# Kernel tuning notes

Hardware: AMD Instinct MI355X
Metric: run time of the kernel (lower is better)

The kernel has to match this reference:

```python
import jax, jax.numpy as jnp
import numpy as np

SEQ = 512      # sentence length n
WD, TD = 100, 28
IN = WD + TD   # 128, lstm input size == hidden size
H = IN         # 128
D = 2 * H      # 256, biLSTM output per token
MLP_IN = 2 * D # 512
HID = MLP_IN   # 512, MLP hidden (hidden_size=mlpInputSize)
V, T = 50000, 50


def setup_inputs() -> dict:
    key = jax.random.key(0)
    keys = iter(jax.random.split(key, 64))
    def nrm(shape, s=0.1):
        return jax.random.normal(next(keys), shape, jnp.float32) * s
    inp = {}
    inp["word_ids"] = jax.random.randint(next(keys), (SEQ,), 0, V)
    inp["tag_ids"] = jax.random.randint(next(keys), (SEQ,), 0, T)
    inp["word_emb_table"] = nrm((V, WD))
    inp["tag_emb_table"] = nrm((T, TD))
    # initHiddenCellState: randn, layout [layer*2+dir, hidden] (batch=1 squeezed)
    inp["h0"] = nrm((4, H), 1.0)
    inp["c0"] = nrm((4, H), 1.0)
    # 2-layer biLSTM params; layer0 input IN, layer1 input 2*H
    for l, insz in ((0, IN), (1, 2 * H)):
        for d in ("f", "b"):
            inp[f"Wih_l{l}{d}"] = nrm((4 * H, insz))
            inp[f"Whh_l{l}{d}"] = nrm((4 * H, H))
            inp[f"bih_l{l}{d}"] = nrm((4 * H,))
            inp[f"bhh_l{l}{d}"] = nrm((4 * H,))
    # MLP: Linear(MLP_IN, HID) -> tanh -> Linear(HID, 1)
    inp["W1"] = nrm((HID, MLP_IN))
    inp["b1"] = nrm((HID,))
    inp["W2"] = nrm((1, HID))
    inp["b2"] = nrm((1,))
    return inp


def _run_dir(x, Wih, Whh, bih, bhh, h0, c0, rev):
    # x: [S, in]; returns hidden states [S, H]
    xs = x[::-1] if rev else x
    pre = xs @ Wih.T + bih + bhh  # precompute input contribution [S, 4H]
    def step(carry, p):
        h, c = carry
        g = p + h @ Whh.T
        i, f, gg, o = jnp.split(g, 4)
        i, f, o = jax.nn.sigmoid(i), jax.nn.sigmoid(f), jax.nn.sigmoid(o)
        c = f * c + i * jnp.tanh(gg)
        h = o * jnp.tanh(c)
        return (h, c), h
    _, hs = jax.lax.scan(step, (h0, c0), pre)
    return hs[::-1] if rev else hs


def reference(word_ids, tag_ids, word_emb_table, tag_emb_table, h0, c0,
              Wih_l0f, Whh_l0f, bih_l0f, bhh_l0f,
              Wih_l0b, Whh_l0b, bih_l0b, bhh_l0b,
              Wih_l1f, Whh_l1f, bih_l1f, bhh_l1f,
              Wih_l1b, Whh_l1b, bih_l1b, bhh_l1b,
              W1, b1, W2, b2):
    # embed + concat: [S, IN]
    x = jnp.concatenate([word_emb_table[word_ids], tag_emb_table[tag_ids]], axis=1)
    layers = [((Wih_l0f, Whh_l0f, bih_l0f, bhh_l0f), (Wih_l0b, Whh_l0b, bih_l0b, bhh_l0b)),
              ((Wih_l1f, Whh_l1f, bih_l1f, bhh_l1f), (Wih_l1b, Whh_l1b, bih_l1b, bhh_l1b))]
    h = x
    for l, (pf, pb) in enumerate(layers):
        hf = _run_dir(h, *pf, h0[2 * l], c0[2 * l], False)
        hb = _run_dir(h, *pb, h0[2 * l + 1], c0[2 * l + 1], True)
        h = jnp.concatenate([hf, hb], axis=1)  # [S, 2H]
    # batched pairwise MLP: score(i,j) = W2 @ tanh(W1 @ [h_i; h_j] + b1) + b2
    W1a, W1b = W1[:, :D], W1[:, D:]
    A = h @ W1a.T  # [S, HID]
    B = h @ W1b.T  # [S, HID]
    hmid = jnp.tanh(A[:, None, :] + B[None, :, :] + b1)  # [S, S, HID]
    scores = jnp.einsum('nmh,h->nm', hmid, W2[0]) + b2[0]
    # diagonal never written in the original (permutations exclude i==i)
    scores = scores * (1.0 - jnp.eye(SEQ, dtype=scores.dtype))
    # column normalization by column sums
    scores = scores / scores.sum(axis=0, keepdims=True)
    # nn.Softmax() on 2D -> dim=1
    return jax.nn.softmax(scores, axis=1)
```

## Files before the change

kernel.cpp:

```cpp
#include <hip/hip_runtime.h>

#define LOG2E 1.4426950408889634f
#define TWO_LOG2E 2.8853900817779268f

#if __has_builtin(__builtin_amdgcn_exp2f)
__device__ __forceinline__ float fexp2(float x){ return __builtin_amdgcn_exp2f(x); }
#else
__device__ __forceinline__ float fexp2(float x){ return exp2f(x); }
#endif
#if __has_builtin(__builtin_amdgcn_rcpf)
__device__ __forceinline__ float frcp(float x){ return __builtin_amdgcn_rcpf(x); }
#else
__device__ __forceinline__ float frcp(float x){ return 1.0f/(x); }
#endif

template<int CTRL>
__device__ __forceinline__ float dpp_f(float x) {
    return __int_as_float(__builtin_amdgcn_update_dpp(0, __float_as_int(x), CTRL, 0xF, 0xF, true));
}
#define DPP_XOR1  0xB1
#define DPP_XOR2  0x4E
#define DPP_BC0   0x00
#define DPP_BC1   0x55
#define DPP_BC2   0xAA
#define DPP_BC3   0xFF

__global__ __launch_bounds__(256) void gemm_l0(
    const int* __restrict__ wid, const int* __restrict__ tgi,
    const float* __restrict__ wemb, const float* __restrict__ temb,
    const float* __restrict__ Wa, const float* __restrict__ Wb,
    const float* __restrict__ b1a, const float* __restrict__ b1b,
    const float* __restrict__ b2a, const float* __restrict__ b2b,
    float* __restrict__ Ca, float* __restrict__ Cb,
    float* __restrict__ csum)
{
    int tid = threadIdx.x;
    if (blockIdx.x == 0 && blockIdx.y == 0 && blockIdx.z == 0) {
        csum[tid] = 0.f; csum[tid + 256] = 0.f;
    }
    int z = blockIdx.z;
    const float* W   = z ? Wb  : Wa;
    const float* bb1 = z ? b1b : b1a;
    const float* bb2 = z ? b2b : b2a;
    float* C = z ? Cb : Ca;

    __shared__ float Xs[64*33];
    __shared__ float Ws[64*33];
    int tx = tid & 15, ty = tid >> 4;
    int n0 = blockIdx.y*64, r0 = blockIdx.x*64;
    float acc[4][4] = {};

    for (int k0 = 0; k0 < 128; k0 += 32) {
        #pragma unroll
        for (int i = 0; i < 2; ++i) {
            int idx = tid + 256*i;
            int row = idx >> 3, c4 = idx & 7;
            int k = k0 + c4*4;
            int rg = n0 + row;
            float4 vx = (k < 100) ? *(const float4*)(wemb + wid[rg]*100 + k)
                                  : *(const float4*)(temb + tgi[rg]*28 + (k-100));
            float4 vw = *(const float4*)(W + (r0+row)*128 + k0 + c4*4);
            Xs[row*33 + c4*4+0]=vx.x; Xs[row*33 + c4*4+1]=vx.y; Xs[row*33 + c4*4+2]=vx.z; Xs[row*33 + c4*4+3]=vx.w;
            Ws[row*33 + c4*4+0]=vw.x; Ws[row*33 + c4*4+1]=vw.y; Ws[row*33 + c4*4+2]=vw.z; Ws[row*33 + c4*4+3]=vw.w;
        }
        __syncthreads();
        #pragma unroll 8
        for (int kk = 0; kk < 32; ++kk) {
            float a[4], b[4];
            #pragma unroll
            for (int i = 0; i < 4; ++i) a[i] = Xs[(4*ty+i)*33 + kk];
            #pragma unroll
            for (int j = 0; j < 4; ++j) b[j] = Ws[(4*tx+j)*33 + kk];
            #pragma unroll
            for (int i = 0; i < 4; ++i)
                #pragma unroll
                for (int j = 0; j < 4; ++j)
                    acc[i][j] = fmaf(a[i], b[j], acc[i][j]);
        }
        __syncthreads();
    }
    #pragma unroll
    for (int i = 0; i < 4; ++i)
        #pragma unroll
        for (int j = 0; j < 4; ++j) {
            int r = r0 + 4*tx + j;
            C[(n0 + 4*ty + i)*512 + r] = acc[i][j] + bb1[r] + bb2[r];
        }
}

__global__ __launch_bounds__(256) void gemm2(
    const float* __restrict__ X, int ldx,
    const float* __restrict__ Wa, const float* __restrict__ Wb, int ldw, int woffb,
    const float* __restrict__ b1a, const float* __restrict__ b1b,
    const float* __restrict__ b2a, const float* __restrict__ b2b,
    float* __restrict__ Ca, float* __restrict__ Cb,
    int K, float scale)
{
    int z = blockIdx.z;
    const float* W  = z ? Wb  : Wa;
    const float* bb1 = z ? b1b : b1a;
    const float* bb2 = z ? b2b : b2a;
    float* C = z ? Cb : Ca;
    int woff = z ? woffb : 0;

    __shared__ float Xs[64*33];
    __shared__ float Ws[64*33];
    int tid = threadIdx.x;
    int tx = tid & 15, ty = tid >> 4;
    int n0 = blockIdx.y*64, r0 = blockIdx.x*64;
    float acc[4][4] = {};

    for (int k0 = 0; k0 < K; k0 += 32) {
        #pragma unroll
        for (int i = 0; i < 2; ++i) {
            int idx = tid + 256*i;
            int row = idx >> 3, c4 = idx & 7;
            float4 vx = *(const float4*)(X + (n0+row)*ldx + k0 + c4*4);
            float4 vw = *(const float4*)(W + (r0+row)*ldw + woff + k0 + c4*4);
            Xs[row*33 + c4*4+0]=vx.x; Xs[row*33 + c4*4+1]=vx.y; Xs[row*33 + c4*4+2]=vx.z; Xs[row*33 + c4*4+3]=vx.w;
            Ws[row*33 + c4*4+0]=vw.x; Ws[row*33 + c4*4+1]=vw.y; Ws[row*33 + c4*4+2]=vw.z; Ws[row*33 + c4*4+3]=vw.w;
        }
        __syncthreads();
        #pragma unroll 8
        for (int kk = 0; kk < 32; ++kk) {
            float a[4], b[4];
            #pragma unroll
            for (int i = 0; i < 4; ++i) a[i] = Xs[(4*ty+i)*33 + kk];
            #pragma unroll
            for (int j = 0; j < 4; ++j) b[j] = Ws[(4*tx+j)*33 + kk];
            #pragma unroll
            for (int i = 0; i < 4; ++i)
                #pragma unroll
                for (int j = 0; j < 4; ++j)
                    acc[i][j] = fmaf(a[i], b[j], acc[i][j]);
        }
        __syncthreads();
    }
    #pragma unroll
    for (int i = 0; i < 4; ++i)
        #pragma unroll
        for (int j = 0; j < 4; ++j) {
            int r = r0 + 4*tx + j;
            float v = acc[i][j];
            if (bb1) v += bb1[r];
            if (bb2) v += bb2[r];
            C[(n0 + 4*ty + i)*512 + r] = v*scale;
        }
}

__global__ __launch_bounds__(512, 2) void lstm_kernel(
    const float* __restrict__ preF, const float* __restrict__ preB,
    const float* __restrict__ WhhF, const float* __restrict__ WhhB,
    const float* __restrict__ h0, const float* __restrict__ c0,
    float* __restrict__ hout, int layer)
{
    const int dir = blockIdx.x;
    const int tid = threadIdx.x;
    const int sub = tid & 3;
    const int j   = tid >> 2;
    const int q   = sub;
    const float* Whh  = dir ? WhhB : WhhF;
    const float* preD = dir ? preB : preF;

    int cidx[8];
    #pragma unroll
    for (int k = 0; k < 8; ++k) cidx[k] = (sub << 3) + ((k + 2*sub) & 7);

    float w[4][32];
    #pragma unroll
    for (int r = 0; r < 4; ++r) {
        const float* wr = Whh + ((r << 7) + j)*128;
        #pragma unroll
        for (int k = 0; k < 8; ++k) {
            float4 v = *(const float4*)(wr + 4*cidx[k]);
            w[r][4*k+0]=v.x; w[r][4*k+1]=v.y; w[r][4*k+2]=v.z; w[r][4*k+3]=v.w;
        }
    }

    __shared__ __align__(16) float hbuf[2][128];

    const float* h0d = h0 + (2*layer + dir)*128;
    const float* c0d = c0 + (2*layer + dir)*128;
    float c = c0d[j];
    if (tid < 128) hbuf[0][tid] = h0d[tid];

    const float sc = (q == 2) ? -TWO_LOG2E : -LOG2E;
    const int prow = (q << 7) + j;
    const int t0 = dir ? 511 : 0;
    const int dt = dir ? -1 : 1;

    float pcur = preD[t0*512 + prow];
    __syncthreads();

    #pragma unroll 2
    for (int s = 0; s < 512; ++s) {
        const int t  = t0 + dt*s;
        const int tn = (s < 511) ? (t + dt) : t;
        float pnext = preD[tn*512 + prow];

        const int p = s & 1;
        const float4* h4 = (const float4*)hbuf[p];
        float4 hv[8];
        #pragma unroll
        for (int k = 0; k < 8; ++k) hv[k] = h4[cidx[k]];

        float acc[4] = {0.f, 0.f, 0.f, 0.f};
        #pragma unroll
        for (int k = 0; k < 8; ++k) {
            #pragma unroll
            for (int r = 0; r < 4; ++r) {
                acc[r] = fmaf(hv[k].x, w[r][4*k+0], acc[r]);
                acc[r] = fmaf(hv[k].y, w[r][4*k+1], acc[r]);
                acc[r] = fmaf(hv[k].z, w[r][4*k+2], acc[r]);
                acc[r] = fmaf(hv[k].w, w[r][4*k+3], acc[r]);
            }
        }

        #pragma unroll
        for (int r = 0; r < 4; ++r) {
            acc[r] += dpp_f<DPP_XOR1>(acc[r]);
            acc[r] += dpp_f<DPP_XOR2>(acc[r]);
        }

        float a01 = (q & 1) ? acc[1] : acc[0];
        float a23 = (q & 1) ? acc[3] : acc[2];
        float xg  = (((q & 2) ? a23 : a01) + pcur) * sc;
        float sv  = frcp(1.f + fexp2(xg));

        float vi = dpp_f<DPP_BC0>(sv);
        float vf = dpp_f<DPP_BC1>(sv);
        float vg = dpp_f<DPP_BC2>(sv);
        float vo = dpp_f<DPP_BC3>(sv);

        float tg = fmaf(2.f, vg, -1.f);
        c = fmaf(vf, c, vi*tg);
        float th = fmaf(-2.f, frcp(1.f + fexp2(TWO_LOG2E*c)), 1.f);
        float h  = vo * th;

        if (sub == 1) hbuf[p ^ 1][j] = h;
        if (sub == 2) hout[t*256 + dir*128 + j] = h;
        __syncthreads();
        pcur = pnext;
    }
}

__global__ __launch_bounds__(256) void score_kernel(
    const float* __restrict__ Ap, const float* __restrict__ Bp,
    const float* __restrict__ W2, const float* __restrict__ b2p,
    float* __restrict__ S, float* __restrict__ csum)
{
    __shared__ __align__(16) float As[32*132];
    __shared__ __align__(16) float Bs[16*132];
    __shared__ __align__(16) float W2s[128];
    __shared__ float ps[16][17];
    int tid = threadIdx.x;
    int tx = tid & 15, ty = tid >> 4;
    int m0 = blockIdx.x*16, n0 = blockIdx.y*32;
    float acc0 = 0.f, acc1 = 0.f;

    for (int hc = 0; hc < 512; hc += 128) {
        #pragma unroll
        for (int i = 0; i < 4; ++i) {
            int idx = tid + 256*i;
            int row = idx >> 5, c4 = idx & 31;
            *(float4*)&As[row*132 + c4*4] = *(const float4*)(Ap + (n0+row)*512 + hc + c4*4);
        }
        #pragma unroll
        for (int i = 0; i < 2; ++i) {
            int idx = tid + 256*i;
            int row = idx >> 5, c4 = idx & 31;
            *(float4*)&Bs[row*132 + c4*4] = *(const float4*)(Bp + (m0+row)*512 + hc + c4*4);
        }
        if (tid < 128) W2s[tid] = W2[hc + tid];
        __syncthreads();

        #pragma unroll 4
        for (int h4 = 0; h4 < 32; ++h4) {
            float4 a0 = *(const float4*)&As[ty*132 + 4*h4];
            float4 a1 = *(const float4*)&As[(ty+16)*132 + 4*h4];
            float4 bv = *(const float4*)&Bs[tx*132 + 4*h4];
            float4 w4 = *(const float4*)&W2s[4*h4];
            float aa0[4] = {a0.x,a0.y,a0.z,a0.w};
            float aa1[4] = {a1.x,a1.y,a1.z,a1.w};
            float bb[4]  = {bv.x,bv.y,bv.z,bv.w};
            float ww[4]  = {w4.x,w4.y,w4.z,w4.w};
            #pragma unroll
            for (int qi = 0; qi < 4; ++qi) {
                float r0v = frcp(1.f + fexp2(aa0[qi] + bb[qi]));
                float r1v = frcp(1.f + fexp2(aa1[qi] + bb[qi]));
                acc0 = fmaf(ww[qi], fmaf(-2.f, r0v, 1.f), acc0);
                acc1 = fmaf(ww[qi], fmaf(-2.f, r1v, 1.f), acc1);
            }
        }
        __syncthreads();
    }

    float b2s = b2p[0];
    int gm  = m0 + tx;
    int gn0 = n0 + ty;
    int gn1 = n0 + 16 + ty;
    float v0 = acc0 + b2s; if (gn0 == gm) v0 = 0.f;
    float v1 = acc1 + b2s; if (gn1 == gm) v1 = 0.f;
    S[gn0*512 + gm] = v0;
    S[gn1*512 + gm] = v1;

    ps[ty][tx] = v0 + v1;
    __syncthreads();
    if (tid < 16) {
        float s = 0.f;
        #pragma unroll
        for (int k = 0; k < 16; ++k) s += ps[k][tid];
        atomicAdd(&csum[m0 + tid], s);
    }
}

__global__ __launch_bounds__(256) void softmax_kernel(const float* __restrict__ S,
                                                      const float* __restrict__ csum,
                                                      float* __restrict__ out)
{
    int n = blockIdx.x, tid = threadIdx.x;
    float v0 = S[n*512 + tid]       / csum[tid];
    float v1 = S[n*512 + tid + 256] / csum[tid + 256];

    __shared__ float rbuf[4], rbuf2[4];
    int wid = tid >> 6;

    float mx = fmaxf(v0, v1);
    #pragma unroll
    for (int off = 32; off; off >>= 1) mx = fmaxf(mx, __shfl_xor(mx, off, 64));
    if ((tid & 63) == 0) rbuf[wid] = mx;
    __syncthreads();
    mx = fmaxf(fmaxf(rbuf[0], rbuf[1]), fmaxf(rbuf[2], rbuf[3]));

    float e0 = fexp2((v0 - mx)*LOG2E);
    float e1 = fexp2((v1 - mx)*LOG2E);
    float sm = e0 + e1;
    #pragma unroll
    for (int off = 32; off; off >>= 1) sm += __shfl_xor(sm, off, 64);
    if ((tid & 63) == 0) rbuf2[wid] = sm;
    __syncthreads();
    sm = (rbuf2[0] + rbuf2[1]) + (rbuf2[2] + rbuf2[3]);

    float inv = 1.0f / sm;
    out[n*512 + tid]       = e0*inv;
    out[n*512 + tid + 256] = e1*inv;
}

extern "C" void kernel_launch(void* const* d_in, const int* in_sizes, int n_in,
                              void* d_out, int out_size, void* d_ws, size_t ws_size,
                              hipStream_t stream)
{
    const int*   wid  = (const int*)d_in[0];
    const int*   tgi  = (const int*)d_in[1];
    const float* wemb = (const float*)d_in[2];
    const float* temb = (const float*)d_in[3];
    const float* h0   = (const float*)d_in[4];
    const float* c0   = (const float*)d_in[5];
    const float* Wih0f=(const float*)d_in[6],  *Whh0f=(const float*)d_in[7],  *bih0f=(const float*)d_in[8],  *bhh0f=(const float*)d_in[9];
    const float* Wih0b=(const float*)d_in[10], *Whh0b=(const float*)d_in[11], *bih0b=(const float*)d_in[12], *bhh0b=(const float*)d_in[13];
    const float* Wih1f=(const float*)d_in[14], *Whh1f=(const float*)d_in[15], *bih1f=(const float*)d_in[16], *bhh1f=(const float*)d_in[17];
    const float* Wih1b=(const float*)d_in[18], *Whh1b=(const float*)d_in[19], *bih1b=(const float*)d_in[20], *bhh1b=(const float*)d_in[21];
    const float* W1   = (const float*)d_in[22];
    const float* b1   = (const float*)d_in[23];
    const float* W2   = (const float*)d_in[24];
    const float* b2   = (const float*)d_in[25];

    float* ws    = (float*)d_ws;
    float* h0cat = ws;
    float* h1cat = ws + 131072;
    float* pA    = ws + 262144;
    float* pB    = ws + 524288;
    float* S     = ws;
    float* csum  = ws + 786432;
    float* out   = (float*)d_out;

    gemm_l0<<<dim3(8,8,2), 256, 0, stream>>>(wid, tgi, wemb, temb,
                                             Wih0f, Wih0b, bih0f, bih0b, bhh0f, bhh0b,
                                             pA, pB, csum);
    lstm_kernel<<<2, 512, 0, stream>>>(pA, pB, Whh0f, Whh0b, h0, c0, h0cat, 0);

    gemm2<<<dim3(8,8,2), 256, 0, stream>>>(h0cat, 256, Wih1f, Wih1b, 256, 0,
                                           bih1f, bih1b, bhh1f, bhh1b,
                                           pA, pB, 256, 1.0f);
    lstm_kernel<<<2, 512, 0, stream>>>(pA, pB, Whh1f, Whh1b, h0, c0, h1cat, 1);

    gemm2<<<dim3(8,8,2), 256, 0, stream>>>(h1cat, 256, W1, W1, 512, 256,
                                           b1, nullptr, nullptr, nullptr,
                                           pA, pB, 256, TWO_LOG2E);

    score_kernel<<<dim3(32,16), 256, 0, stream>>>(pA, pB, W2, b2, S, csum);
    softmax_kernel<<<512, 256, 0, stream>>>(S, csum, out);
}
```

Baseline: 757.1 us.

## Remap LSTM recurrence to eight lanes per hidden-unit pair

The LSTM step kernel now gives each 8-lane group two hidden units. Each lane holds 8 gate rows by 16 columns of Whh instead of 4 rows by 32 columns. This halves the per-step LDS reads of the hidden state per thread, which matters on the serial critical path. In exchange, each step needs a third DPP reduction stage (row half-mirror) across 8 accumulators, so cross-lane work per step roughly triples.

```diff
diff --git a/kernel.cpp b/kernel.cpp
--- a/kernel.cpp
+++ b/kernel.cpp
@@ -20,6 +20,7 @@
 }
 #define DPP_XOR1  0xB1
 #define DPP_XOR2  0x4E
+#define DPP_HMIR  0x141
 #define DPP_BC0   0x00
 #define DPP_BC1   0x55
 #define DPP_BC2   0xAA
@@ -156,36 +157,41 @@
 {
     const int dir = blockIdx.x;
     const int tid = threadIdx.x;
-    const int sub = tid & 3;
-    const int j   = tid >> 2;
-    const int q   = sub;
+    const int sub = tid & 7;
+    const int g   = tid >> 3;
+    const int j0  = 2*g;
+    const int qown = sub & 3;
+    const int cown = sub >> 2;
     const float* Whh  = dir ? WhhB : WhhF;
     const float* preD = dir ? preB : preF;
 
-    int cidx[8];
-    #pragma unroll
-    for (int k = 0; k < 8; ++k) cidx[k] = (sub << 3) + ((k + 2*sub) & 7);
-
-    float w[4][32];
-    #pragma unroll
-    for (int r = 0; r < 4; ++r) {
-        const float* wr = Whh + ((r << 7) + j)*128;
-        #pragma unroll
-        for (int k = 0; k < 8; ++k) {
-            float4 v = *(const float4*)(wr + 4*cidx[k]);
-            w[r][4*k+0]=v.x; w[r][4*k+1]=v.y; w[r][4*k+2]=v.z; w[r][4*k+3]=v.w;
-        }
-    }
+    int cidx[4];
+    #pragma unroll
+    for (int k = 0; k < 4; ++k) cidx[k] = (sub << 2) + ((k + sub) & 3);
+
+    float w[8][16];
+    #pragma unroll
+    for (int cc = 0; cc < 2; ++cc)
+        #pragma unroll
+        for (int qq = 0; qq < 4; ++qq) {
+            const float* wr = Whh + ((qq << 7) + j0 + cc)*128;
+            #pragma unroll
+            for (int k = 0; k < 4; ++k) {
+                float4 v = *(const float4*)(wr + 4*cidx[k]);
+                int r = (cc << 2) | qq;
+                w[r][4*k+0]=v.x; w[r][4*k+1]=v.y; w[r][4*k+2]=v.z; w[r][4*k+3]=v.w;
+            }
+        }
 
     __shared__ __align__(16) float hbuf[2][128];
 
     const float* h0d = h0 + (2*layer + dir)*128;
     const float* c0d = c0 + (2*layer + dir)*128;
-    float c = c0d[j];
+    float c = c0d[j0 + cown];
     if (tid < 128) hbuf[0][tid] = h0d[tid];
 
-    const float sc = (q == 2) ? -TWO_LOG2E : -LOG2E;
-    const int prow = (q << 7) + j;
+    const float sc = (qown == 2) ? -TWO_LOG2E : -LOG2E;
+    const int prow = (qown << 7) + j0 + cown;
     const int t0 = dir ? 511 : 0;
     const int dt = dir ? -1 : 1;
 
@@ -200,15 +206,15 @@
 
         const int p = s & 1;
         const float4* h4 = (const float4*)hbuf[p];
-        float4 hv[8];
-        #pragma unroll
-        for (int k = 0; k < 8; ++k) hv[k] = h4[cidx[k]];
-
-        float acc[4] = {0.f, 0.f, 0.f, 0.f};
-        #pragma unroll
-        for (int k = 0; k < 8; ++k) {
-            #pragma unroll
-            for (int r = 0; r < 4; ++r) {
+        float4 hv[4];
+        #pragma unroll
+        for (int k = 0; k < 4; ++k) hv[k] = h4[cidx[k]];
+
+        float acc[8] = {0.f,0.f,0.f,0.f,0.f,0.f,0.f,0.f};
+        #pragma unroll
+        for (int k = 0; k < 4; ++k) {
+            #pragma unroll
+            for (int r = 0; r < 8; ++r) {
                 acc[r] = fmaf(hv[k].x, w[r][4*k+0], acc[r]);
                 acc[r] = fmaf(hv[k].y, w[r][4*k+1], acc[r]);
                 acc[r] = fmaf(hv[k].z, w[r][4*k+2], acc[r]);
@@ -217,15 +223,20 @@
         }
 
         #pragma unroll
-        for (int r = 0; r < 4; ++r) {
+        for (int r = 0; r < 8; ++r) {
             acc[r] += dpp_f<DPP_XOR1>(acc[r]);
             acc[r] += dpp_f<DPP_XOR2>(acc[r]);
-        }
-
-        float a01 = (q & 1) ? acc[1] : acc[0];
-        float a23 = (q & 1) ? acc[3] : acc[2];
-        float xg  = (((q & 2) ? a23 : a01) + pcur) * sc;
-        float sv  = frcp(1.f + fexp2(xg));
+            acc[r] += dpp_f<DPP_HMIR>(acc[r]);
+        }
+
+        float a0 = (sub & 4) ? acc[4] : acc[0];
+        float a1 = (sub & 4) ? acc[5] : acc[1];
+        float a2 = (sub & 4) ? acc[6] : acc[2];
+        float a3 = (sub & 4) ? acc[7] : acc[3];
+        float t01 = (sub & 1) ? a1 : a0;
+        float t23 = (sub & 1) ? a3 : a2;
+        float x   = ((sub & 2) ? t23 : t01) + pcur;
+        float sv  = frcp(1.f + fexp2(x * sc));
 
         float vi = dpp_f<DPP_BC0>(sv);
         float vf = dpp_f<DPP_BC1>(sv);
@@ -237,8 +248,10 @@
         float th = fmaf(-2.f, frcp(1.f + fexp2(TWO_LOG2E*c)), 1.f);
         float h  = vo * th;
 
-        if (sub == 1) hbuf[p ^ 1][j] = h;
-        if (sub == 2) hout[t*256 + dir*128 + j] = h;
+        if (sub == 1) hbuf[p ^ 1][j0] = h;
+        if (sub == 5) hbuf[p ^ 1][j0 + 1] = h;
+        if (sub == 2) hout[t*256 + dir*128 + j0] = h;
+        if (sub == 6) hout[t*256 + dir*128 + j0 + 1] = h;
         __syncthreads();
         pcur = pnext;
     }
```

After: 923.3 us. +22.0%, slower.

## Fuse all stages into one cooperative persistent kernel with grid syncs

Applied to the files above, without the earlier changes.

Replaces the seven separate kernel launches (three GEMMs, two LSTM recurrences, score and softmax) with a single cooperative kernel of 256 blocks of 512 threads. Stages are separated by grid-wide syncs, and each stage maps its work onto block indices, so the GEMM tiles now use 512 threads with 2x4 outputs each. The aim is to remove launch and inter-kernel gaps, which matter because the LSTM stages run on only two blocks. In exchange, most blocks sit idle during the long LSTM phases, and the kernel pays grid-sync costs plus higher register and shared-memory pressure from one merged kernel.

```diff
diff --git a/kernel.cpp b/kernel.cpp
--- a/kernel.cpp
+++ b/kernel.cpp
@@ -1,4 +1,7 @@
 #include <hip/hip_runtime.h>
+#include <hip/hip_cooperative_groups.h>
+
+namespace cg = cooperative_groups;
 
 #define LOG2E 1.4426950408889634f
 #define TWO_LOG2E 2.8853900817779268f
@@ -25,142 +28,72 @@
 #define DPP_BC2   0xAA
 #define DPP_BC3   0xFF
 
-__global__ __launch_bounds__(256) void gemm_l0(
+#define SM_FLOATS 13472
+
+template<bool L0>
+__device__ __forceinline__ void gemm_tile(
+    float* __restrict__ Xs, float* __restrict__ Ws, int tid,
+    const float* __restrict__ X, int ldx,
+    const float* __restrict__ W, int ldw, int woff,
+    const float* __restrict__ bb1, const float* __restrict__ bb2,
+    float* __restrict__ C, int n0, int r0, int K, float scale,
     const int* __restrict__ wid, const int* __restrict__ tgi,
-    const float* __restrict__ wemb, const float* __restrict__ temb,
-    const float* __restrict__ Wa, const float* __restrict__ Wb,
-    const float* __restrict__ b1a, const float* __restrict__ b1b,
-    const float* __restrict__ b2a, const float* __restrict__ b2b,
-    float* __restrict__ Ca, float* __restrict__ Cb,
-    float* __restrict__ csum)
-{
-    int tid = threadIdx.x;
-    if (blockIdx.x == 0 && blockIdx.y == 0 && blockIdx.z == 0) {
-        csum[tid] = 0.f; csum[tid + 256] = 0.f;
-    }
-    int z = blockIdx.z;
-    const float* W   = z ? Wb  : Wa;
-    const float* bb1 = z ? b1b : b1a;
-    const float* bb2 = z ? b2b : b2a;
-    float* C = z ? Cb : Ca;
-
-    __shared__ float Xs[64*33];
-    __shared__ float Ws[64*33];
+    const float* __restrict__ wemb, const float* __restrict__ temb)
+{
     int tx = tid & 15, ty = tid >> 4;
-    int n0 = blockIdx.y*64, r0 = blockIdx.x*64;
-    float acc[4][4] = {};
-
-    for (int k0 = 0; k0 < 128; k0 += 32) {
-        #pragma unroll
-        for (int i = 0; i < 2; ++i) {
-            int idx = tid + 256*i;
-            int row = idx >> 3, c4 = idx & 7;
-            int k = k0 + c4*4;
+    int row = tid >> 3, c4 = tid & 7;
+    float acc[2][4] = {};
+    for (int k0 = 0; k0 < K; k0 += 32) {
+        int k = k0 + c4*4;
+        float4 vx, vw;
+        if (L0) {
             int rg = n0 + row;
-            float4 vx = (k < 100) ? *(const float4*)(wemb + wid[rg]*100 + k)
-                                  : *(const float4*)(temb + tgi[rg]*28 + (k-100));
-            float4 vw = *(const float4*)(W + (r0+row)*128 + k0 + c4*4);
-            Xs[row*33 + c4*4+0]=vx.x; Xs[row*33 + c4*4+1]=vx.y; Xs[row*33 + c4*4+2]=vx.z; Xs[row*33 + c4*4+3]=vx.w;
-            Ws[row*33 + c4*4+0]=vw.x; Ws[row*33 + c4*4+1]=vw.y; Ws[row*33 + c4*4+2]=vw.z; Ws[row*33 + c4*4+3]=vw.w;
-        }
+            vx = (k < 100) ? *(const float4*)(wemb + wid[rg]*100 + k)
+                           : *(const float4*)(temb + tgi[rg]*28 + (k-100));
+            vw = *(const float4*)(W + (r0+row)*128 + k);
+        } else {
+            vx = *(const float4*)(X + (n0+row)*ldx + k);
+            vw = *(const float4*)(W + (r0+row)*ldw + woff + k);
+        }
+        Xs[row*33 + c4*4+0]=vx.x; Xs[row*33 + c4*4+1]=vx.y; Xs[row*33 + c4*4+2]=vx.z; Xs[row*33 + c4*4+3]=vx.w;
+        Ws[row*33 + c4*4+0]=vw.x; Ws[row*33 + c4*4+1]=vw.y; Ws[row*33 + c4*4+2]=vw.z; Ws[row*33 + c4*4+3]=vw.w;
         __syncthreads();
         #pragma unroll 8
         for (int kk = 0; kk < 32; ++kk) {
-            float a[4], b[4];
+            float a0 = Xs[(2*ty)*33 + kk];
+            float a1 = Xs[(2*ty+1)*33 + kk];
+            float bv[4];
             #pragma unroll
-            for (int i = 0; i < 4; ++i) a[i] = Xs[(4*ty+i)*33 + kk];
+            for (int jj = 0; jj < 4; ++jj) bv[jj] = Ws[(4*tx+jj)*33 + kk];
             #pragma unroll
-            for (int j = 0; j < 4; ++j) b[j] = Ws[(4*tx+j)*33 + kk];
-            #pragma unroll
-            for (int i = 0; i < 4; ++i)
-                #pragma unroll
-                for (int j = 0; j < 4; ++j)
-                    acc[i][j] = fmaf(a[i], b[j], acc[i][j]);
-        }
-        __syncthreads();
-    }
-    #pragma unroll
-    for (int i = 0; i < 4; ++i)
-        #pragma unroll
-        for (int j = 0; j < 4; ++j) {
-            int r = r0 + 4*tx + j;
-            C[(n0 + 4*ty + i)*512 + r] = acc[i][j] + bb1[r] + bb2[r];
-        }
-}
-
-__global__ __launch_bounds__(256) void gemm2(
-    const float* __restrict__ X, int ldx,
-    const float* __restrict__ Wa, const float* __restrict__ Wb, int ldw, int woffb,
-    const float* __restrict__ b1a, const float* __restrict__ b1b,
-    const float* __restrict__ b2a, const float* __restrict__ b2b,
-    float* __restrict__ Ca, float* __restrict__ Cb,
-    int K, float scale)
-{
-    int z = blockIdx.z;
-    const float* W  = z ? Wb  : Wa;
-    const float* bb1 = z ? b1b : b1a;
-    const float* bb2 = z ? b2b : b2a;
-    float* C = z ? Cb : Ca;
-    int woff = z ? woffb : 0;
-
-    __shared__ float Xs[64*33];
-    __shared__ float Ws[64*33];
-    int tid = threadIdx.x;
-    int tx = tid & 15, ty = tid >> 4;
-    int n0 = blockIdx.y*64, r0 = blockIdx.x*64;
-    float acc[4][4] = {};
-
-    for (int k0 = 0; k0 < K; k0 += 32) {
-        #pragma unroll
-        for (int i = 0; i < 2; ++i) {
-            int idx = tid + 256*i;
-            int row = idx >> 3, c4 = idx & 7;
-            float4 vx = *(const float4*)(X + (n0+row)*ldx + k0 + c4*4);
-            float4 vw = *(const float4*)(W + (r0+row)*ldw + woff + k0 + c4*4);
-            Xs[row*33 + c4*4+0]=vx.x; Xs[row*33 + c4*4+1]=vx.y; Xs[row*33 + c4*4+2]=vx.z; Xs[row*33 + c4*4+3]=vx.w;
-            Ws[row*33 + c4*4+0]=vw.x; Ws[row*33 + c4*4+1]=vw.y; Ws[row*33 + c4*4+2]=vw.z; Ws[row*33 + c4*4+3]=vw.w;
-        }
-        __syncthreads();
-        #pragma unroll 8
-        for (int kk = 0; kk < 32; ++kk) {
-            float a[4], b[4];
-            #pragma unroll
-            for (int i = 0; i < 4; ++i) a[i] = Xs[(4*ty+i)*33 + kk];
-            #pragma unroll
-            for (int j = 0; j < 4; ++j) b[j] = Ws[(4*tx+j)*33 + kk];
-            #pragma unroll
-            for (int i = 0; i < 4; ++i)
-                #pragma unroll
-                for (int j = 0; j < 4; ++j)
-                    acc[i][j] = fmaf(a[i], b[j], acc[i][j]);
-        }
-        __syncthreads();
-    }
-    #pragma unroll
-    for (int i = 0; i < 4; ++i)
-        #pragma unroll
-        for (int j = 0; j < 4; ++j) {
-            int r = r0 + 4*tx + j;
-            float v = acc[i][j];
+            for (int jj = 0; jj < 4; ++jj) {
+                acc[0][jj] = fmaf(a0, bv[jj], acc[0][jj]);
+                acc[1][jj] = fmaf(a1, bv[jj], acc[1][jj]);
+            }
+        }
+        __syncthreads();
+    }
+    #pragma unroll
+    for (int i = 0; i < 2; ++i)
+        #pragma unroll
+        for (int jj = 0; jj < 4; ++jj) {
+            int r = r0 + 4*tx + jj;
+            float v = acc[i][jj];
             if (bb1) v += bb1[r];
             if (bb2) v += bb2[r];
-            C[(n0 + 4*ty + i)*512 + r] = v*scale;
-        }
-}
-
-__global__ __launch_bounds__(512, 2) void lstm_kernel(
-    const float* __restrict__ preF, const float* __restrict__ preB,
-    const float* __restrict__ WhhF, const float* __restrict__ WhhB,
+            C[(n0 + 2*ty + i)*512 + r] = v*scale;
+        }
+}
+
+__device__ __forceinline__ void lstm_body(
+    float* hbuf, int tid, int dir, int layer,
+    const float* __restrict__ preD, const float* __restrict__ Whh,
     const float* __restrict__ h0, const float* __restrict__ c0,
-    float* __restrict__ hout, int layer)
-{
-    const int dir = blockIdx.x;
-    const int tid = threadIdx.x;
+    float* hout)
+{
     const int sub = tid & 3;
     const int j   = tid >> 2;
     const int q   = sub;
-    const float* Whh  = dir ? WhhB : WhhF;
-    const float* preD = dir ? preB : preF;
 
     int cidx[8];
     #pragma unroll
@@ -177,12 +110,10 @@
         }
     }
 
-    __shared__ __align__(16) float hbuf[2][128];
-
     const float* h0d = h0 + (2*layer + dir)*128;
     const float* c0d = c0 + (2*layer + dir)*128;
     float c = c0d[j];
-    if (tid < 128) hbuf[0][tid] = h0d[tid];
+    if (tid < 128) hbuf[tid] = h0d[tid];
 
     const float sc = (q == 2) ? -TWO_LOG2E : -LOG2E;
     const int prow = (q << 7) + j;
@@ -199,7 +130,7 @@
         float pnext = preD[tn*512 + prow];
 
         const int p = s & 1;
-        const float4* h4 = (const float4*)hbuf[p];
+        const float4* h4 = (const float4*)(hbuf + p*128);
         float4 hv[8];
         #pragma unroll
         for (int k = 0; k < 8; ++k) hv[k] = h4[cidx[k]];
@@ -237,49 +168,44 @@
         float th = fmaf(-2.f, frcp(1.f + fexp2(TWO_LOG2E*c)), 1.f);
         float h  = vo * th;
 
-        if (sub == 1) hbuf[p ^ 1][j] = h;
+        if (sub == 1) hbuf[(p ^ 1)*128 + j] = h;
         if (sub == 2) hout[t*256 + dir*128 + j] = h;
         __syncthreads();
         pcur = pnext;
     }
 }
 
-__global__ __launch_bounds__(256) void score_kernel(
+__device__ __forceinline__ void score_tile(
+    float* __restrict__ As, float* __restrict__ Bs,
+    float* __restrict__ W2s, float* __restrict__ ps, int t,
     const float* __restrict__ Ap, const float* __restrict__ Bp,
     const float* __restrict__ W2, const float* __restrict__ b2p,
-    float* __restrict__ S, float* __restrict__ csum)
-{
-    __shared__ __align__(16) float As[32*132];
-    __shared__ __align__(16) float Bs[16*132];
-    __shared__ __align__(16) float W2s[128];
-    __shared__ float ps[16][17];
-    int tid = threadIdx.x;
-    int tx = tid & 15, ty = tid >> 4;
-    int m0 = blockIdx.x*16, n0 = blockIdx.y*32;
+    float* S, float* csum, int m0, int n0)
+{
+    int tx = t & 15, ty = t >> 4;
     float acc0 = 0.f, acc1 = 0.f;
-
     for (int hc = 0; hc < 512; hc += 128) {
         #pragma unroll
         for (int i = 0; i < 4; ++i) {
-            int idx = tid + 256*i;
+            int idx = t + 256*i;
             int row = idx >> 5, c4 = idx & 31;
             *(float4*)&As[row*132 + c4*4] = *(const float4*)(Ap + (n0+row)*512 + hc + c4*4);
         }
         #pragma unroll
         for (int i = 0; i < 2; ++i) {
-            int idx = tid + 256*i;
+            int idx = t + 256*i;
             int row = idx >> 5, c4 = idx & 31;
             *(float4*)&Bs[row*132 + c4*4] = *(const float4*)(Bp + (m0+row)*512 + hc + c4*4);
         }
-        if (tid < 128) W2s[tid] = W2[hc + tid];
+        if (t < 128) W2s[t] = W2[hc + t];
         __syncthreads();
 
         #pragma unroll 4
-        for (int h4 = 0; h4 < 32; ++h4) {
-            float4 a0 = *(const float4*)&As[ty*132 + 4*h4];
-            float4 a1 = *(const float4*)&As[(ty+16)*132 + 4*h4];
-            float4 bv = *(const float4*)&Bs[tx*132 + 4*h4];
-            float4 w4 = *(const float4*)&W2s[4*h4];
+        for (int h4i = 0; h4i < 32; ++h4i) {
+            float4 a0 = *(const float4*)&As[ty*132 + 4*h4i];
+            float4 a1 = *(const float4*)&As[(ty+16)*132 + 4*h4i];
+            float4 bv = *(const float4*)&Bs[tx*132 + 4*h4i];
+            float4 w4 = *(const float4*)&W2s[4*h4i];
             float aa0[4] = {a0.x,a0.y,a0.z,a0.w};
             float aa1[4] = {a1.x,a1.y,a1.z,a1.w};
             float bb[4]  = {bv.x,bv.y,bv.z,bv.w};
@@ -304,46 +230,127 @@
     S[gn0*512 + gm] = v0;
     S[gn1*512 + gm] = v1;
 
-    ps[ty][tx] = v0 + v1;
-    __syncthreads();
-    if (tid < 16) {
+    ps[ty*17 + tx] = v0 + v1;
+    __syncthreads();
+    if (t < 16) {
         float s = 0.f;
         #pragma unroll
-        for (int k = 0; k < 16; ++k) s += ps[k][tid];
-        atomicAdd(&csum[m0 + tid], s);
-    }
-}
-
-__global__ __launch_bounds__(256) void softmax_kernel(const float* __restrict__ S,
-                                                      const float* __restrict__ csum,
-                                                      float* __restrict__ out)
-{
-    int n = blockIdx.x, tid = threadIdx.x;
-    float v0 = S[n*512 + tid]       / csum[tid];
-    float v1 = S[n*512 + tid + 256] / csum[tid + 256];
-
-    __shared__ float rbuf[4], rbuf2[4];
-    int wid = tid >> 6;
-
-    float mx = fmaxf(v0, v1);
+        for (int k = 0; k < 16; ++k) s += ps[k*17 + t];
+        atomicAdd(&csum[m0 + t], s);
+    }
+}
+
+__device__ __forceinline__ void softmax_row(
+    int n, int tid, float* rbuf, float* rbuf2,
+    const float* S, const float* __restrict__ csum, float* __restrict__ out)
+{
+    float v = S[n*512 + tid] / csum[tid];
+    int lane = tid & 63, wv = tid >> 6;
+    float mx = v;
     #pragma unroll
     for (int off = 32; off; off >>= 1) mx = fmaxf(mx, __shfl_xor(mx, off, 64));
-    if ((tid & 63) == 0) rbuf[wid] = mx;
-    __syncthreads();
-    mx = fmaxf(fmaxf(rbuf[0], rbuf[1]), fmaxf(rbuf[2], rbuf[3]));
-
-    float e0 = fexp2((v0 - mx)*LOG2E);
-    float e1 = fexp2((v1 - mx)*LOG2E);
-    float sm = e0 + e1;
+    if (lane == 0) rbuf[wv] = mx;
+    __syncthreads();
+    mx = rbuf[0];
+    #pragma unroll
+    for (int k = 1; k < 8; ++k) mx = fmaxf(mx, rbuf[k]);
+
+    float e = fexp2((v - mx)*LOG2E);
+    float sm = e;
     #pragma unroll
     for (int off = 32; off; off >>= 1) sm += __shfl_xor(sm, off, 64);
-    if ((tid & 63) == 0) rbuf2[wid] = sm;
-    __syncthreads();
-    sm = (rbuf2[0] + rbuf2[1]) + (rbuf2[2] + rbuf2[3]);
-
-    float inv = 1.0f / sm;
-    out[n*512 + tid]       = e0*inv;
-    out[n*512 + tid + 256] = e1*inv;
+    if (lane == 0) rbuf2[wv] = sm;
+    __syncthreads();
+    float tot = rbuf2[0];
+    #pragma unroll
+    for (int k = 1; k < 8; ++k) tot += rbuf2[k];
+
+    float inv = 1.0f / tot;
+    out[n*512 + tid] = e*inv;
+}
+
+__global__ __launch_bounds__(512, 2) void fused(
+    const int* __restrict__ wid, const int* __restrict__ tgi,
+    const float* __restrict__ wemb, const float* __restrict__ temb,
+    const float* __restrict__ h0, const float* __restrict__ c0,
+    const float* __restrict__ Wih0f, const float* __restrict__ Whh0f,
+    const float* __restrict__ bih0f, const float* __restrict__ bhh0f,
+    const float* __restrict__ Wih0b, const float* __restrict__ Whh0b,
+    const float* __restrict__ bih0b, const float* __restrict__ bhh0b,
+    const float* __restrict__ Wih1f, const float* __restrict__ Whh1f,
+    const float* __restrict__ bih1f, const float* __restrict__ bhh1f,
+    const float* __restrict__ Wih1b, const float* __restrict__ Whh1b,
+    const float* __restrict__ bih1b, const float* __restrict__ bhh1b,
+    const float* __restrict__ W1, const float* __restrict__ b1,
+    const float* __restrict__ W2, const float* __restrict__ b2,
+    float* h0cat, float* h1cat,
+    float* pA, float* pB,
+    float* S, float* csum, float* out)
+{
+    __shared__ __align__(16) float smem[SM_FLOATS];
+    cg::grid_group grid = cg::this_grid();
+    const int b = blockIdx.x;
+    const int tid = threadIdx.x;
+
+    if (b < 128) {
+        int z = b >> 6, rem = b & 63;
+        gemm_tile<true>(smem, smem + 2112, tid,
+                        nullptr, 0, z ? Wih0b : Wih0f, 128, 0,
+                        z ? bih0b : bih0f, z ? bhh0b : bhh0f,
+                        z ? pB : pA, (rem >> 3)*64, (rem & 7)*64, 128, 1.0f,
+                        wid, tgi, wemb, temb);
+    } else if (b == 128) {
+        csum[tid] = 0.f;
+    }
+    __threadfence();
+    grid.sync();
+
+    if (b < 2)
+        lstm_body(smem, tid, b, 0, b ? pB : pA, b ? Whh0b : Whh0f, h0, c0, h0cat);
+    __threadfence();
+    grid.sync();
+
+    if (b < 128) {
+        int z = b >> 6, rem = b & 63;
+        gemm_tile<false>(smem, smem + 2112, tid,
+                         h0cat, 256, z ? Wih1b : Wih1f, 256, 0,
+                         z ? bih1b : bih1f, z ? bhh1b : bhh1f,
+                         z ? pB : pA, (rem >> 3)*64, (rem & 7)*64, 256, 1.0f,
+                         nullptr, nullptr, nullptr, nullptr);
+    }
+    __threadfence();
+    grid.sync();
+
+    if (b < 2)
+        lstm_body(smem, tid, b, 1, b ? pB : pA, b ? Whh1b : Whh1f, h0, c0, h1cat);
+    __threadfence();
+    grid.sync();
+
+    if (b < 128) {
+        int z = b >> 6, rem = b & 63;
+        gemm_tile<false>(smem, smem + 2112, tid,
+                         h1cat, 256, W1, 512, z ? 256 : 0,
+                         z ? nullptr : b1, nullptr,
+                         z ? pB : pA, (rem >> 3)*64, (rem & 7)*64, 256, TWO_LOG2E,
+                         nullptr, nullptr, nullptr, nullptr);
+    }
+    __threadfence();
+    grid.sync();
+
+    {
+        int half = tid >> 8, t = tid & 255;
+        int tile = 2*b + half;
+        int m0 = (tile & 31) * 16, n0 = (tile >> 5) * 32;
+        float* base = smem + half*6736;
+        score_tile(base, base + 4224, base + 6336, base + 6464, t,
+                   pA, pB, W2, b2, S, csum, m0, n0);
+    }
+    __threadfence();
+    grid.sync();
+
+    softmax_row(b, tid, smem, smem + 8, S, csum, out);
+    __syncthreads();
+    softmax_row(b + 256, tid, smem, smem + 8, S, csum, out);
 }
 
 extern "C" void kernel_launch(void* const* d_in, const int* in_sizes, int n_in,
@@ -374,20 +381,16 @@
     float* csum  = ws + 786432;
     float* out   = (float*)d_out;
 
-    gemm_l0<<<dim3(8,8,2), 256, 0, stream>>>(wid, tgi, wemb, temb,
-                                             Wih0f, Wih0b, bih0f, bih0b, bhh0f, bhh0b,
-                                             pA, pB, csum);
-    lstm_kernel<<<2, 512, 0, stream>>>(pA, pB, Whh0f, Whh0b, h0, c0, h0cat, 0);
-
-    gemm2<<<dim3(8,8,2), 256, 0, stream>>>(h0cat, 256, Wih1f, Wih1b, 256, 0,
-                                           bih1f, bih1b, bhh1f, bhh1b,
-                                           pA, pB, 256, 1.0f);
-    lstm_kernel<<<2, 512, 0, stream>>>(pA, pB, Whh1f, Whh1b, h0, c0, h1cat, 1);
-
-    gemm2<<<dim3(8,8,2), 256, 0, stream>>>(h1cat, 256, W1, W1, 512, 256,
-                                           b1, nullptr, nullptr, nullptr,
-                                           pA, pB, 256, TWO_LOG2E);
-
-    score_kernel<<<dim3(32,16), 256, 0, stream>>>(pA, pB, W2, b2, S, csum);
-    softmax_kernel<<<512, 256, 0, stream>>>(S, csum, out);
-}
+    void* kargs[] = {
+        (void*)&wid, (void*)&tgi, (void*)&wemb, (void*)&temb,
+        (void*)&h0, (void*)&c0,
+        (void*)&Wih0f, (void*)&Whh0f, (void*)&bih0f, (void*)&bhh0f,
+        (void*)&Wih0b, (void*)&Whh0b, (void*)&bih0b, (void*)&bhh0b,
+        (void*)&Wih1f, (void*)&Whh1f, (void*)&bih1f, (void*)&bhh1f,
+        (void*)&Wih1b, (void*)&Whh1b, (void*)&bih1b, (void*)&bhh1b,
+        (void*)&W1, (void*)&b1, (void*)&W2, (void*)&b2,
+        (void*)&h0cat, (void*)&h1cat, (void*)&pA, (void*)&pB,
+        (void*)&S, (void*)&csum, (void*)&out
+    };
+    hipLaunchCooperativeKernel(fused, dim3(256), dim3(512), kargs, 0, stream);
+}
```

New measurement: 1.174 ms. +55.0%, slower.
